# Kernel tuning notes

Hardware: AMD Instinct MI355X
Metric: run time of the kernel (lower is better)

## Reference

```python
import jax, jax.numpy as jnp
import numpy as np

K = 3  # neighbors for knn_interpolate


def _knn_interpolate(x, pos, pos_skip, B, k):
    """PyG knn_interpolate with equal-sized batches.
    x: [N_coarse, C], pos: [N_coarse, 3], pos_skip: [N_fine, 3].
    """
    C = x.shape[1]
    xb = x.reshape(B, -1, C)          # [B, nc, C]
    pb = pos.reshape(B, -1, 3)        # [B, nc, 3]
    qb = pos_skip.reshape(B, -1, 3)   # [B, nf, 3]

    def per_cloud(xf, pf, qf):
        # squared distances [nf, nc]
        d2 = jnp.sum((qf[:, None, :] - pf[None, :, :]) ** 2, axis=-1)
        neg_d2k, idx = jax.lax.top_k(-d2, k)          # k smallest distances
        d2k = -neg_d2k                                # [nf, k]
        w = 1.0 / jnp.clip(d2k, 1e-16)                # inverse-distance weights
        w = jax.lax.stop_gradient(w)                  # PyG computes weights under no_grad
        feats = xf[idx]                               # [nf, k, C] gather
        return jnp.sum(w[..., None] * feats, axis=1) / jnp.sum(w, axis=1, keepdims=True)

    y = jax.vmap(per_cloud)(xb, pb, qb)               # [B, nf, C]
    return y.reshape(-1, C)


def setup_inputs() -> dict:
    key = jax.random.key(0)
    ks = jax.random.split(key, 8)
    B, n_coarse, n_fine = 16, 1024, 4096
    C_in, C_skip, C_mid, C_out = 256, 128, 256, 256
    x = jax.random.normal(ks[0], (B * n_coarse, C_in), jnp.float32)
    pos = jax.random.uniform(ks[1], (B * n_coarse, 3), jnp.float32)
    x_skip = jax.random.normal(ks[2], (B * n_fine, C_skip), jnp.float32)
    pos_skip = jax.random.uniform(ks[3], (B * n_fine, 3), jnp.float32)
    batch = jnp.repeat(jnp.arange(B, dtype=jnp.int64), n_coarse)
    batch_skip = jnp.repeat(jnp.arange(B, dtype=jnp.int64), n_fine)
    seed_idx = jnp.arange(B * n_coarse, dtype=jnp.int64)
    seed_idx_skip = jnp.arange(B * n_fine, dtype=jnp.int64)
    W1 = jax.random.normal(ks[4], (C_in + C_skip, C_mid), jnp.float32) * 0.05
    b1 = jnp.zeros((C_mid,), jnp.float32)
    W2 = jax.random.normal(ks[5], (C_mid, C_out), jnp.float32) * 0.05
    b2 = jnp.zeros((C_out,), jnp.float32)
    return {"x": x, "pos": pos, "batch": batch, "seed_idx": seed_idx,
            "x_skip": x_skip, "pos_skip": pos_skip, "batch_skip": batch_skip,
            "seed_idx_skip": seed_idx_skip, "W1": W1, "b1": b1, "W2": W2, "b2": b2}


def reference(x, pos, batch, seed_idx, x_skip, pos_skip, batch_skip, seed_idx_skip,
              W1, b1, W2, b2):
    B = int(batch[-1]) + 1  # equal-sized contiguous clouds
    y = _knn_interpolate(x, pos, pos_skip, B, K)      # [N_fine, C_in]
    h = jnp.concatenate([y, x_skip], axis=1)          # [N_fine, C_in+C_skip]
    h = jax.nn.relu(h @ W1 + b1)                      # MLP layer 1
    out = jax.nn.relu(h @ W2 + b2)                    # MLP layer 2
    return (out, pos_skip, batch_skip)
```

## Files before the change

kernel.cpp:

```cpp
#include <hip/hip_runtime.h>
#include <hip/hip_bf16.h>

#define NB    16
#define NC    1024
#define NF    4096
#define NFINE (NB*NF)
#define CIN   256
#define CSKIP 128
#define KH    (CIN+CSKIP)
#define CMID  256
#define COUT  256

typedef __attribute__((ext_vector_type(8))) short short8;
typedef __attribute__((ext_vector_type(4))) float f32x4;
typedef __attribute__((ext_vector_type(4))) unsigned int u32x4;

__device__ __forceinline__ float bf2f(short s) {
    return __uint_as_float(((unsigned)(unsigned short)s) << 16);
}

__global__ __launch_bounds__(256)
void bin_kernel(const float* __restrict__ pos,
                float* __restrict__ gp,
                int* __restrict__ gcs)
{
    __shared__ int cnt[512];
    __shared__ float lx[NC], ly[NC], lz[NC];
    __shared__ short lcell[NC];
    const int b = blockIdx.x, t = threadIdx.x;
    for (int i = t; i < 512; i += 256) cnt[i] = 0;
    __syncthreads();
    const float* pc = pos + (size_t)b*NC*3;
    #pragma unroll
    for (int u = 0; u < 4; ++u) {
        int i = t + u*256;
        float x = pc[3*i+0], y = pc[3*i+1], z = pc[3*i+2];
        int cx = min(7, (int)(x*8.0f));
        int cy = min(7, (int)(y*8.0f));
        int cz = min(7, (int)(z*8.0f));
        int c = (cz*8 + cy)*8 + cx;
        lx[i] = x; ly[i] = y; lz[i] = z; lcell[i] = (short)c;
        atomicAdd(&cnt[c], 1);
    }
    __syncthreads();
    if (t < 64) {
        int v[8]; int s = 0;
        #pragma unroll
        for (int u = 0; u < 8; ++u) { v[u] = cnt[t*8+u]; s += v[u]; }
        int pfx = s;
        #pragma unroll
        for (int m = 1; m < 64; m <<= 1) {
            int o = __shfl_up(pfx, m);
            if (t >= m) pfx += o;
        }
        pfx -= s;
        #pragma unroll
        for (int u = 0; u < 8; ++u) {
            gcs[b*513 + t*8+u] = pfx;
            cnt[t*8+u] = pfx;
            pfx += v[u];
        }
        if (t == 63) gcs[b*513 + 512] = NC;
    }
    __syncthreads();
    #pragma unroll
    for (int u = 0; u < 4; ++u) {
        int i = t + u*256;
        int c = lcell[i];
        int dst = atomicAdd(&cnt[c], 1);
        f32x4 v; v[0] = lx[i]; v[1] = ly[i]; v[2] = lz[i]; v[3] = __int_as_float(i);
        *(f32x4*)&gp[(size_t)(b*NC + dst)*4] = v;
    }
}

#define KQPB 64

#define INS(d, j) do {                                        \
    bool c2 = (d) < dB, c1 = (d) < dA, c0 = (d) < d0;         \
    dB = c1 ? dA : (c2 ? (d) : dB);                           \
    iB = c1 ? iA : (c2 ? (j) : iB);                           \
    dA = c0 ? d0 : (c1 ? (d) : dA);                           \
    iA = c0 ? i0 : (c1 ? (j) : iA);                           \
    d0 = c0 ? (d) : d0;                                       \
    i0 = c0 ? (j) : i0;                                       \
} while (0)

#define SCAN(JS, JE) for (int j = (JS) + g; j < (JE); j += 8) {        \
    const f32x4 p = *(const f32x4*)&pp[j][0];                          \
    float fx = qx - p[0], fy = qy - p[1], fz = qz - p[2];              \
    float dd = fx*fx + fy*fy + fz*fz;                                  \
    INS(dd, j);                                                        \
}

#define MERGE8() do {                                                          \
    _Pragma("unroll")                                                          \
    for (int mm = 1; mm < 8; mm <<= 1) {                                       \
        float e0 = __shfl_xor(d0, mm), e1 = __shfl_xor(dA, mm), e2 = __shfl_xor(dB, mm); \
        int   f0 = __shfl_xor(i0, mm), f1 = __shfl_xor(iA, mm), f2 = __shfl_xor(iB, mm); \
        INS(e0, f0); INS(e1, f1); INS(e2, f2);                                 \
    }                                                                          \
} while (0)

__global__ __launch_bounds__(512)
void knn_grid_kernel(const float* __restrict__ pos_skip,
                     const float* __restrict__ gp,
                     const int* __restrict__ gcs,
                     int* __restrict__ widx, float* __restrict__ wval,
                     float* __restrict__ out)
{
    __shared__ __align__(16) float pp[NC][4];
    __shared__ unsigned short cs[513];
    const int bpc = NF/KQPB;
    const int b  = blockIdx.x / bpc;
    const int qb = blockIdx.x % bpc;
    const int t  = threadIdx.x;

    {
        int e = blockIdx.x*192 + t;
        if (t < 192) out[(size_t)NFINE*COUT + e] = pos_skip[e];
        if (t >= 192 && t < 256) {
            int e2 = blockIdx.x*64 + (t - 192);
            out[(size_t)NFINE*COUT + (size_t)NFINE*3 + e2] = (float)(e2 >> 12);
        }
    }

    for (int i = t; i < NC; i += 512)
        *(f32x4*)&pp[i][0] = *(const f32x4*)&gp[(size_t)(b*NC + i)*4];
    for (int i = t; i < 513; i += 512) cs[i] = (unsigned short)gcs[b*513 + i];
    __syncthreads();

    const int g  = t & 7;
    const int ql = t >> 3;
    const int q  = b*NF + qb*KQPB + ql;
    const float qx = pos_skip[(size_t)q*3+0];
    const float qy = pos_skip[(size_t)q*3+1];
    const float qz = pos_skip[(size_t)q*3+2];
    const int cx = min(7, (int)(qx*8.0f));
    const int cy = min(7, (int)(qy*8.0f));
    const int cz = min(7, (int)(qz*8.0f));

    float d0 = 3.0e38f, dA = 3.0e38f, dB = 3.0e38f;
    int   i0 = 0,       iA = 0,       iB = 0;

    const int xlo = max(cx-1,0), xhi = min(cx+1,7);
    const int ylo = max(cy-1,0), yhi = min(cy+1,7);
    const int zlo = max(cz-1,0), zhi = min(cz+1,7);
    #pragma unroll
    for (int r = 0; r < 9; ++r) {
        const int z = cz - 1 + r/3;
        const int y = cy - 1 + r%3;
        const bool ok = ((unsigned)z < 8u) & ((unsigned)y < 8u);
        const int rb = (z*8 + y)*8;
        int js = 0, je = 0;
        if (ok) { js = cs[rb + xlo]; je = cs[rb + xhi + 1]; }
        SCAN(js, je);
    }
    MERGE8();

    float m1 = 3.0e38f;
    if (xlo > 0) m1 = fminf(m1, qx - xlo*0.125f);
    if (xhi < 7) m1 = fminf(m1, (xhi+1)*0.125f - qx);
    if (ylo > 0) m1 = fminf(m1, qy - ylo*0.125f);
    if (yhi < 7) m1 = fminf(m1, (yhi+1)*0.125f - qy);
    if (zlo > 0) m1 = fminf(m1, qz - zlo*0.125f);
    if (zhi < 7) m1 = fminf(m1, (zhi+1)*0.125f - qz);

    if (dB > m1*m1) {
        const float s0 = d0, s1 = dA, s2 = dB;
        const int   t0 = i0, t1 = iA, t2 = iB;
        d0 = dA = dB = 3.0e38f; i0 = iA = iB = 0;

        const int xlo2 = max(cx-2,0), xhi2 = min(cx+2,7);
        const int ylo2 = max(cy-2,0), yhi2 = min(cy+2,7);
        const int zlo2 = max(cz-2,0), zhi2 = min(cz+2,7);
        for (int z = zlo2; z <= zhi2; ++z)
        for (int y = ylo2; y <= yhi2; ++y) {
            const int rb = (z*8 + y)*8;
            const bool inner_zy = (z >= zlo && z <= zhi && y >= ylo && y <= yhi);
            int jsA, jeA, jsB, jeB;
            if (inner_zy) {
                jsA = cs[rb + xlo2]; jeA = cs[rb + xlo];
                jsB = cs[rb + xhi + 1]; jeB = cs[rb + xhi2 + 1];
            } else {
                jsA = cs[rb + xlo2]; jeA = cs[rb + xhi2 + 1];
                jsB = 0; jeB = 0;
            }
            SCAN(jsA, jeA);
            SCAN(jsB, jeB);
        }
        MERGE8();
        INS(s0, t0); INS(s1, t1); INS(s2, t2);

        float m2 = 3.0e38f;
        if (xlo2 > 0) m2 = fminf(m2, qx - xlo2*0.125f);
        if (xhi2 < 7) m2 = fminf(m2, (xhi2+1)*0.125f - qx);
        if (ylo2 > 0) m2 = fminf(m2, qy - ylo2*0.125f);
        if (yhi2 < 7) m2 = fminf(m2, (yhi2+1)*0.125f - qy);
        if (zlo2 > 0) m2 = fminf(m2, qz - zlo2*0.125f);
        if (zhi2 < 7) m2 = fminf(m2, (zhi2+1)*0.125f - qz);
        if (dB > m2*m2) {
            const float u0 = d0, u1 = dA, u2 = dB;
            const int   v0 = i0, v1 = iA, v2 = iB;
            d0 = dA = dB = 3.0e38f; i0 = iA = iB = 0;
            for (int j = g; j < NC; j += 8) {
                const f32x4 p = *(const f32x4*)&pp[j][0];
                int pcx = min(7, (int)(p[0]*8.0f));
                int pcy = min(7, (int)(p[1]*8.0f));
                int pcz = min(7, (int)(p[2]*8.0f));
                if (pcx >= xlo2 && pcx <= xhi2 && pcy >= ylo2 && pcy <= yhi2 &&
                    pcz >= zlo2 && pcz <= zhi2) continue;
                float fx = qx - p[0], fy = qy - p[1], fz = qz - p[2];
                float dd = fx*fx + fy*fy + fz*fz;
                INS(dd, j);
            }
            MERGE8();
            INS(u0, v0); INS(u1, v1); INS(u2, v2);
        }
    }

    if (g == 0) {
        const int o0 = __float_as_int(pp[i0][3]);
        const int o1 = __float_as_int(pp[iA][3]);
        const int o2 = __float_as_int(pp[iB][3]);
        float w0 = 1.0f / fmaxf(d0, 1e-16f);
        float w1 = 1.0f / fmaxf(dA, 1e-16f);
        float w2 = 1.0f / fmaxf(dB, 1e-16f);
        float inv = 1.0f / (w0 + w1 + w2);
        widx[q*3+0] = b*NC + o0;  wval[q*3+0] = w0*inv;
        widx[q*3+1] = b*NC + o1;  wval[q*3+1] = w1*inv;
        widx[q*3+2] = b*NC + o2;  wval[q*3+2] = w2*inv;
    }
}

__global__ __launch_bounds__(256)
void prep_weights(const float* __restrict__ W1, const float* __restrict__ W2,
                  __hip_bfloat16* __restrict__ W1at,
                  __hip_bfloat16* __restrict__ imgG,
                  __hip_bfloat16* __restrict__ img2)
{
    int e = blockIdx.x*256 + threadIdx.x;
    if (e < CMID*CIN) {
        int n = e / CIN, k = e % CIN;
        W1at[e] = __float2bfloat16(W1[(size_t)k*CMID + n]);
    }
    int e2 = e - CMID*CIN;
    if (e2 >= 0 && e2 < 2*2048*8) {
        int chunk = e2 >> 3, el = e2 & 7;
        int s = chunk >> 11, L = chunk & 2047;
        int rr = L >> 3, sl = L & 7;
        int k = s*64 + ((sl ^ (rr & 7)) << 3) + el;
        imgG[e2] = __float2bfloat16(W1[(size_t)(CIN + k)*CMID + rr]);
    }
    int e3 = e2 - 2*2048*8;
    if (e3 >= 0 && e3 < 4*2048*8) {
        int chunk = e3 >> 3, el = e3 & 7;
        int s = chunk >> 11, L = chunk & 2047;
        int rr = L >> 3, sl = L & 7;
        int k = s*64 + ((sl ^ (rr & 7)) << 3) + el;
        img2[e3] = __float2bfloat16(W2[(size_t)k*COUT + rr]);
    }
}

__global__ __launch_bounds__(512, 2)
void gemmZ_kernel(const float* __restrict__ x,
                  const __hip_bfloat16* __restrict__ W1at,
                  __hip_bfloat16* __restrict__ Z)
{
    __shared__ __align__(16) short As[64][64];
    __shared__ __align__(16) short Bs[256][64];
    const int m0 = blockIdx.x * 64;

    const int t = threadIdx.x;
    const int wave = t >> 6, lane = t & 63;
    const int wm = wave >> 2, wn = wave & 3;
    const int rl = lane & 15, kq = lane >> 4;
    const short* Br = (const short*)W1at;

    const int ar = t >> 3;
    const int ac = t & 7;

    f32x4 rA[2];
    u32x4 rB[4];

    #define LOADAZ(K0) do {                                                    \
        const float* p = &x[(size_t)(m0+ar)*CIN + (K0) + ac*8];                \
        rA[0] = *(const f32x4*)p; rA[1] = *(const f32x4*)(p+4);                \
    } while (0)
    #define LOADBZ(K0) do {                                                    \
        _Pragma("unroll")                                                      \
        for (int i = 0; i < 4; ++i) {                                          \
            const int ch = t + i*512;                                          \
            const int rr = ch >> 3, cc = ch & 7;                               \
            rB[i] = *(const u32x4*)&Br[(size_t)rr*CIN + (K0) + cc*8];          \
        }                                                                      \
    } while (0)

    f32x4 acc[2][4] = {};
    LOADAZ(0); LOADBZ(0);

    #pragma unroll
    for (int s = 0; s < 4; ++s) {
        __syncthreads();
        {
            short8 sv;
            #pragma unroll
            for (int u = 0; u < 2; ++u) {
                f32x4 a = rA[u];
                #pragma unroll
                for (int e = 0; e < 4; ++e) {
                    __hip_bfloat16 bb = __float2bfloat16(a[e]);
                    ((short*)&sv)[u*4+e] = *(short*)&bb;
                }
            }
            *(short8*)&As[ar][(ac ^ (ar&7))*8] = sv;
        }
        #pragma unroll
        for (int i = 0; i < 4; ++i) {
            const int ch = t + i*512;
            const int rr = ch >> 3, cc = ch & 7;
            *(u32x4*)&Bs[rr][(cc ^ (rr&7))*8] = rB[i];
        }
        __syncthreads();
        if (s < 3) { LOADAZ((s+1)*64); LOADBZ((s+1)*64); }
        #pragma unroll
        for (int kh = 0; kh < 2; ++kh) {
            const int kc = kh*4 + kq;
            short8 af[2], bf[4];
            #pragma unroll
            for (int mf = 0; mf < 2; ++mf)
                af[mf] = *(const short8*)&As[wm*32 + mf*16 + rl][(kc ^ (rl&7))*8];
            #pragma unroll
            for (int nf = 0; nf < 4; ++nf)
                bf[nf] = *(const short8*)&Bs[wn*64 + nf*16 + rl][(kc ^ (rl&7))*8];
            #pragma unroll
            for (int mf = 0; mf < 2; ++mf)
            #pragma unroll
            for (int nf = 0; nf < 4; ++nf)
                acc[mf][nf] = __builtin_amdgcn_mfma_f32_16x16x32_bf16(af[mf], bf[nf], acc[mf][nf], 0,0,0);
        }
    }
    #undef LOADAZ
    #undef LOADBZ

    #pragma unroll
    for (int mf = 0; mf < 2; ++mf)
    #pragma unroll
    for (int nf = 0; nf < 4; ++nf) {
        const int col = wn*64 + nf*16 + rl;
        #pragma unroll
        for (int i = 0; i < 4; ++i) {
            const int row = m0 + wm*32 + mf*16 + kq*4 + i;
            Z[(size_t)row*CMID + col] = __float2bfloat16(acc[mf][nf][i]);
        }
    }
}

__global__ __launch_bounds__(512, 2)
void g2_fused(const float* __restrict__ x_skip,
              const float* __restrict__ b1,
              const __hip_bfloat16* __restrict__ Z,
              const int* __restrict__ widx,
              const float* __restrict__ wval,
              const __hip_bfloat16* __restrict__ imgG,
              const __hip_bfloat16* __restrict__ img2,
              const float* __restrict__ b2,
              float* __restrict__ out)
{
    __shared__ __align__(16) short As[64][128];
    __shared__ __align__(16) short Bs[256][64];
    __shared__ __align__(16) short Hs[64][256];
    const int nwg = gridDim.x;
    const int tile = (blockIdx.x & 7)*(nwg >> 3) + (blockIdx.x >> 3);
    const int m0 = tile * 64;

    const int t = threadIdx.x;
    const int wave = t >> 6, lane = t & 63;
    const int wm = wave >> 2, wn = wave & 3;
    const int rl = lane & 15, kq = lane >> 4;
    const short* gI = (const short*)imgG;
    const short* g2i = (const short*)img2;
    const short* Zr  = (const short*)Z;
    short* BsLin = &Bs[0][0];
    short (*BsH)[64] = (short(*)[64])&Hs[0][0];

    const int ar = t >> 3;
    const int ac = t & 7;

    const float* xs = &x_skip[(size_t)(m0+ar)*CSKIP];
    f32x4 pa0 = *(const f32x4*)&xs[ac*8];
    f32x4 pa1 = *(const f32x4*)&xs[ac*8+4];
    f32x4 pb0 = *(const f32x4*)&xs[64+ac*8];
    f32x4 pb1 = *(const f32x4*)&xs[64+ac*8+4];
    u32x4 rG0[4], rG1[4];
    #pragma unroll
    for (int i = 0; i < 4; ++i) {
        rG0[i] = *(const u32x4*)&gI[(size_t)(       i*512 + t)*8];
        rG1[i] = *(const u32x4*)&gI[(size_t)(2048 + i*512 + t)*8];
    }

    {
        short8 sv0, sv1;
        #pragma unroll
        for (int u = 0; u < 2; ++u) {
            f32x4 a = (u == 0) ? pa0 : pa1;
            f32x4 b = (u == 0) ? pb0 : pb1;
            #pragma unroll
            for (int e = 0; e < 4; ++e) {
                __hip_bfloat16 ba = __float2bfloat16(a[e]);
                __hip_bfloat16 bb = __float2bfloat16(b[e]);
                ((short*)&sv0)[u*4+e] = *(short*)&ba;
                ((short*)&sv1)[u*4+e] = *(short*)&bb;
            }
        }
        const int sw = ac ^ (ar & 7);
        *(short8*)&As[ar][sw*8]     = sv0;
        *(short8*)&As[ar][(8+sw)*8] = sv1;
    }
    #pragma unroll
    for (int i = 0; i < 4; ++i) {
        *(u32x4*)&BsLin[(size_t)(i*512 + t)*8]     = rG0[i];
        *(u32x4*)&(&Hs[0][0])[(size_t)(i*512 + t)*8] = rG1[i];
    }
    __syncthreads();

    f32x4 acc[2][4] = {};
    #pragma unroll
    for (int kh = 0; kh < 2; ++kh) {
        const int kc = kh*4 + kq;
        short8 af[2], bf[4];
        #pragma unroll
        for (int mf = 0; mf < 2; ++mf)
            af[mf] = *(const short8*)&As[wm*32 + mf*16 + rl][((kc ^ (rl&7)))*8];
        #pragma unroll
        for (int nf = 0; nf < 4; ++nf)
            bf[nf] = *(const short8*)&Bs[wn*64 + nf*16 + rl][(kc ^ (rl&7))*8];
        #pragma unroll
        for (int mf = 0; mf < 2; ++mf)
        #pragma unroll
        for (int nf = 0; nf < 4; ++nf)
            acc[mf][nf] = __builtin_amdgcn_mfma_f32_16x16x32_bf16(af[mf], bf[nf], acc[mf][nf], 0,0,0);
    }
    #pragma unroll
    for (int kh = 0; kh < 2; ++kh) {
        const int kc = kh*4 + kq;
        short8 af[2], bf[4];
        #pragma unroll
        for (int mf = 0; mf < 2; ++mf)
            af[mf] = *(const short8*)&As[wm*32 + mf*16 + rl][(8 + (kc ^ (rl&7)))*8];
        #pragma unroll
        for (int nf = 0; nf < 4; ++nf)
            bf[nf] = *(const short8*)&BsH[wn*64 + nf*16 + rl][(kc ^ (rl&7))*8];
        #pragma unroll
        for (int mf = 0; mf < 2; ++mf)
        #pragma unroll
        for (int nf = 0; nf < 4; ++nf)
            acc[mf][nf] = __builtin_amdgcn_mfma_f32_16x16x32_bf16(af[mf], bf[nf], acc[mf][nf], 0,0,0);
    }
    __syncthreads();

    u32x4 rB[4];
    #pragma unroll
    for (int i = 0; i < 4; ++i)
        rB[i] = *(const u32x4*)&g2i[(size_t)(i*512 + t)*8];
    #pragma unroll
    for (int mf = 0; mf < 2; ++mf)
    #pragma unroll
    for (int nf = 0; nf < 4; ++nf) {
        const int col = wn*64 + nf*16 + rl;
        const float bv = b1[col];
        #pragma unroll
        for (int i = 0; i < 4; ++i) {
            const int row = wm*32 + mf*16 + kq*4 + i;
            float v = acc[mf][nf][i] + bv;
            __hip_bfloat16 bb = __float2bfloat16(v);
            Hs[row][((col >> 3) ^ (row & 7))*8 + (col & 7)] = *(short*)&bb;
        }
    }
    #pragma unroll
    for (int i = 0; i < 4; ++i)
        *(u32x4*)&BsLin[(size_t)(i*512 + t)*8] = rB[i];
    __syncthreads();

    #pragma unroll
    for (int u = 0; u < 4; ++u) {
        const int ch = t + u*512;
        const int row = ch >> 5;
        const int cc  = ch & 31;
        const int c   = cc * 8;
        const int gr = (m0 + row)*3;
        const int j0 = widx[gr+0], j1 = widx[gr+1], j2 = widx[gr+2];
        const float w0 = wval[gr+0], w1 = wval[gr+1], w2 = wval[gr+2];
        const short8 z0 = *(const short8*)&Zr[(size_t)j0*CMID + c];
        const short8 z1 = *(const short8*)&Zr[(size_t)j1*CMID + c];
        const short8 z2 = *(const short8*)&Zr[(size_t)j2*CMID + c];
        const int slot = (cc ^ (row & 7))*8;
        short8 gchunk = *(const short8*)&Hs[row][slot];
        short8 r;
        #pragma unroll
        for (int e = 0; e < 8; ++e) {
            float v = bf2f(gchunk[e]) + w0*bf2f(z0[e]) + w1*bf2f(z1[e]) + w2*bf2f(z2[e]);
            v = fmaxf(v, 0.0f);
            __hip_bfloat16 bb = __float2bfloat16(v);
            r[e] = *(short*)&bb;
        }
        *(short8*)&Hs[row][slot] = r;
    }
    __syncthreads();

    f32x4 acc2[2][4] = {};
    #define MFMA2(S2) do {                                                     \
        _Pragma("unroll")                                                      \
        for (int kh = 0; kh < 2; ++kh) {                                       \
            const int kcl = kh*4 + kq;                                         \
            const int kca = (S2)*8 + kcl;                                      \
            short8 af[2], bf[4];                                               \
            _Pragma("unroll")                                                  \
            for (int mf = 0; mf < 2; ++mf)                                     \
                af[mf] = *(const short8*)&Hs[wm*32 + mf*16 + rl][(kca ^ (rl&7))*8]; \
            _Pragma("unroll")                                                  \
            for (int nf = 0; nf < 4; ++nf)                                     \
                bf[nf] = *(const short8*)&Bs[wn*64 + nf*16 + rl][(kcl ^ (rl&7))*8]; \
            _Pragma("unroll")                                                  \
            for (int mf = 0; mf < 2; ++mf)                                     \
            _Pragma("unroll")                                                  \
            for (int nf = 0; nf < 4; ++nf)                                     \
                acc2[mf][nf] = __builtin_amdgcn_mfma_f32_16x16x32_bf16(af[mf], bf[nf], acc2[mf][nf], 0,0,0); \
        }                                                                      \
    } while (0)
    #define LOADI2(S) do {                                                     \
        _Pragma("unroll")                                                      \
        for (int i = 0; i < 4; ++i)                                            \
            rB[i] = *(const u32x4*)&g2i[(size_t)((S)*2048 + i*512 + t)*8];     \
    } while (0)
    #define STAGEI2() do {                                                     \
        _Pragma("unroll")                                                      \
        for (int i = 0; i < 4; ++i)                                            \
            *(u32x4*)&BsLin[(size_t)(i*512 + t)*8] = rB[i];                    \
    } while (0)

    LOADI2(1);
    MFMA2(0);
    __syncthreads();
    STAGEI2();
    __syncthreads();
    LOADI2(2);
    MFMA2(1);
    __syncthreads();
    STAGEI2();
    __syncthreads();
    LOADI2(3);
    MFMA2(2);
    __syncthreads();
    STAGEI2();
    __syncthreads();
    MFMA2(3);

    #pragma unroll
    for (int mf = 0; mf < 2; ++mf)
    #pragma unroll
    for (int nf = 0; nf < 4; ++nf) {
        const int col = wn*64 + nf*16 + rl;
        const float bv = b2[col];
        #pragma unroll
        for (int i = 0; i < 4; ++i) {
            const int row = m0 + wm*32 + mf*16 + kq*4 + i;
            out[(size_t)row*COUT + col] = fmaxf(acc2[mf][nf][i] + bv, 0.0f);
        }
    }
    #undef MFMA2
    #undef LOADI2
    #undef STAGEI2
}

extern "C" void kernel_launch(void* const* d_in, const int* in_sizes, int n_in,
                              void* d_out, int out_size, void* d_ws, size_t ws_size,
                              hipStream_t stream) {
    const float* x        = (const float*)d_in[0];
    const float* pos      = (const float*)d_in[1];
    const float* x_skip   = (const float*)d_in[4];
    const float* pos_skip = (const float*)d_in[5];
    const float* W1       = (const float*)d_in[8];
    const float* b1       = (const float*)d_in[9];
    const float* W2       = (const float*)d_in[10];
    const float* b2       = (const float*)d_in[11];
    float* out = (float*)d_out;
    char* ws = (char*)d_ws;

    int*            widx = (int*)  (ws + 0);
    float*          wval = (float*)(ws + 786432);
    __hip_bfloat16* W1at = (__hip_bfloat16*)(ws + 1572864);
    __hip_bfloat16* imgG = (__hip_bfloat16*)(ws + 1703936);
    __hip_bfloat16* img2 = (__hip_bfloat16*)(ws + 1769472);
    float*          gp   = (float*)(ws + 1900544);
    int*            gcs  = (int*)  (ws + 2162688);
    __hip_bfloat16* Z    = (__hip_bfloat16*)(ws + 2195520);

    hipLaunchKernelGGL(bin_kernel, dim3(NB), dim3(256), 0, stream,
                       pos, gp, gcs);
    hipLaunchKernelGGL(knn_grid_kernel, dim3(NB*(NF/KQPB)), dim3(512), 0, stream,
                       pos_skip, gp, gcs, widx, wval, out);
    hipLaunchKernelGGL(prep_weights, dim3((CMID*CIN + 2*2048*8 + 4*2048*8 + 255)/256), dim3(256), 0, stream,
                       W1, W2, W1at, imgG, img2);
    hipLaunchKernelGGL(gemmZ_kernel, dim3((NB*NC)/64), dim3(512), 0, stream,
                       x, W1at, Z);
    hipLaunchKernelGGL(g2_fused, dim3(NFINE/64), dim3(512), 0, stream,
                       x_skip, b1, Z, widx, wval, imgG, img2, b2, out);
}
```

Baseline: 72.81 us.

## Merge bin+weight prep and knn+Z-GEMM into horizontally fused kernels

```diff
diff --git a/kernel.cpp b/kernel.cpp
--- a/kernel.cpp
+++ b/kernel.cpp
@@ -20,14 +20,42 @@
 }
 
 __global__ __launch_bounds__(256)
-void bin_kernel(const float* __restrict__ pos,
-                float* __restrict__ gp,
-                int* __restrict__ gcs)
+void binprep_kernel(const float* __restrict__ pos,
+                    float* __restrict__ gp, int* __restrict__ gcs,
+                    const float* __restrict__ W1, const float* __restrict__ W2,
+                    __hip_bfloat16* __restrict__ W1at,
+                    __hip_bfloat16* __restrict__ imgG,
+                    __hip_bfloat16* __restrict__ img2)
 {
     __shared__ int cnt[512];
     __shared__ float lx[NC], ly[NC], lz[NC];
     __shared__ short lcell[NC];
-    const int b = blockIdx.x, t = threadIdx.x;
+    const int t = threadIdx.x;
+    if (blockIdx.x >= NB) {
+        int e = (blockIdx.x - NB)*256 + t;
+        if (e < CMID*CIN) {
+            int n = e / CIN, k = e % CIN;
+            W1at[e] = __float2bfloat16(W1[(size_t)k*CMID + n]);
+        }
+        int e2 = e - CMID*CIN;
+        if (e2 >= 0 && e2 < 2*2048*8) {
+            int chunk = e2 >> 3, el = e2 & 7;
+            int s = chunk >> 11, L = chunk & 2047;
+            int rr = L >> 3, sl = L & 7;
+            int k = s*64 + ((sl ^ (rr & 7)) << 3) + el;
+            imgG[e2] = __float2bfloat16(W1[(size_t)(CIN + k)*CMID + rr]);
+        }
+        int e3 = e2 - 2*2048*8;
+        if (e3 >= 0 && e3 < 4*2048*8) {
+            int chunk = e3 >> 3, el = e3 & 7;
+            int s = chunk >> 11, L = chunk & 2047;
+            int rr = L >> 3, sl = L & 7;
+            int k = s*64 + ((sl ^ (rr & 7)) << 3) + el;
+            img2[e3] = __float2bfloat16(W2[(size_t)k*COUT + rr]);
+        }
+        return;
+    }
+    const int b = blockIdx.x;
     for (int i = t; i < 512; i += 256) cnt[i] = 0;
     __syncthreads();
     const float* pc = pos + (size_t)b*NC*3;
@@ -101,19 +129,112 @@
     }                                                                          \
 } while (0)
 
-__global__ __launch_bounds__(512)
-void knn_grid_kernel(const float* __restrict__ pos_skip,
-                     const float* __restrict__ gp,
-                     const int* __restrict__ gcs,
-                     int* __restrict__ widx, float* __restrict__ wval,
-                     float* __restrict__ out)
+union KZMem {
+    struct { float pp[NC][4]; unsigned short cs[513]; } k;
+    struct { short As[64][64]; short Bs[256][64]; } z;
+};
+
+__global__ __launch_bounds__(512, 2)
+void knnZ_kernel(const float* __restrict__ pos_skip,
+                 const float* __restrict__ gp,
+                 const int* __restrict__ gcs,
+                 int* __restrict__ widx, float* __restrict__ wval,
+                 float* __restrict__ out,
+                 const float* __restrict__ x,
+                 const __hip_bfloat16* __restrict__ W1at,
+                 __hip_bfloat16* __restrict__ Z)
 {
-    __shared__ __align__(16) float pp[NC][4];
-    __shared__ unsigned short cs[513];
+    __shared__ __align__(16) KZMem sm;
+    const int t = threadIdx.x;
+
+    if (blockIdx.x >= 1024) {
+        const int m0 = (blockIdx.x - 1024) * 64;
+        const int wave = t >> 6, lane = t & 63;
+        const int wm = wave >> 2, wn = wave & 3;
+        const int rl = lane & 15, kq = lane >> 4;
+        const short* Br = (const short*)W1at;
+        const int ar = t >> 3;
+        const int ac = t & 7;
+        f32x4 rA[2];
+        u32x4 rB[4];
+
+        #define LOADAZ(K0) do {                                                \
+            const float* p = &x[(size_t)(m0+ar)*CIN + (K0) + ac*8];            \
+            rA[0] = *(const f32x4*)p; rA[1] = *(const f32x4*)(p+4);            \
+        } while (0)
+        #define LOADBZ(K0) do {                                                \
+            _Pragma("unroll")                                                  \
+            for (int i = 0; i < 4; ++i) {                                      \
+                const int ch = t + i*512;                                      \
+                const int rr = ch >> 3, cc = ch & 7;                           \
+                rB[i] = *(const u32x4*)&Br[(size_t)rr*CIN + (K0) + cc*8];      \
+            }                                                                  \
+        } while (0)
+
+        f32x4 acc[2][4] = {};
+        LOADAZ(0); LOADBZ(0);
+        #pragma unroll
+        for (int s = 0; s < 4; ++s) {
+            __syncthreads();
+            {
+                short8 sv;
+                #pragma unroll
+                for (int u = 0; u < 2; ++u) {
+                    f32x4 a = rA[u];
+                    #pragma unroll
+                    for (int e = 0; e < 4; ++e) {
+                        __hip_bfloat16 bb = __float2bfloat16(a[e]);
+                        ((short*)&sv)[u*4+e] = *(short*)&bb;
+                    }
+                }
+                *(short8*)&sm.z.As[ar][(ac ^ (ar&7))*8] = sv;
+            }
+            #pragma unroll
+            for (int i = 0; i < 4; ++i) {
+                const int ch = t + i*512;
+                const int rr = ch >> 3, cc = ch & 7;
+                *(u32x4*)&sm.z.Bs[rr][(cc ^ (rr&7))*8] = rB[i];
+            }
+            __syncthreads();
+            if (s < 3) { LOADAZ((s+1)*64); LOADBZ((s+1)*64); }
+            #pragma unroll
+            for (int kh = 0; kh < 2; ++kh) {
+                const int kc = kh*4 + kq;
+                short8 af[2], bf[4];
+                #pragma unroll
+                for (int mf = 0; mf < 2; ++mf)
+                    af[mf] = *(const short8*)&sm.z.As[wm*32 + mf*16 + rl][(kc ^ (rl&7))*8];
+                #pragma unroll
+                for (int nf = 0; nf < 4; ++nf)
+                    bf[nf] = *(const short8*)&sm.z.Bs[wn*64 + nf*16 + rl][(kc ^ (rl&7))*8];
+                #pragma unroll
+                for (int mf = 0; mf < 2; ++mf)
+                #pragma unroll
+                for (int nf = 0; nf < 4; ++nf)
+                    acc[mf][nf] = __builtin_amdgcn_mfma_f32_16x16x32_bf16(af[mf], bf[nf], acc[mf][nf], 0,0,0);
+            }
+        }
+        #undef LOADAZ
+        #undef LOADBZ
+        #pragma unroll
+        for (int mf = 0; mf < 2; ++mf)
+        #pragma unroll
+        for (int nf = 0; nf < 4; ++nf) {
+            const int col = wn*64 + nf*16 + rl;
+            #pragma unroll
+            for (int i = 0; i < 4; ++i) {
+                const int row = m0 + wm*32 + mf*16 + kq*4 + i;
+                Z[(size_t)row*CMID + col] = __float2bfloat16(acc[mf][nf][i]);
+            }
+        }
+        return;
+    }
+
+    float (*pp)[4] = sm.k.pp;
+    unsigned short* cs = sm.k.cs;
     const int bpc = NF/KQPB;
     const int b  = blockIdx.x / bpc;
     const int qb = blockIdx.x % bpc;
-    const int t  = threadIdx.x;
 
     {
         int e = blockIdx.x*192 + t;
@@ -169,7 +290,6 @@
         const float s0 = d0, s1 = dA, s2 = dB;
         const int   t0 = i0, t1 = iA, t2 = iB;
         d0 = dA = dB = 3.0e38f; i0 = iA = iB = 0;
-
         const int xlo2 = max(cx-2,0), xhi2 = min(cx+2,7);
         const int ylo2 = max(cy-2,0), yhi2 = min(cy+2,7);
         const int zlo2 = max(cz-2,0), zhi2 = min(cz+2,7);
@@ -232,129 +352,6 @@
     }
 }
 
-__global__ __launch_bounds__(256)
-void prep_weights(const float* __restrict__ W1, const float* __restrict__ W2,
-                  __hip_bfloat16* __restrict__ W1at,
-                  __hip_bfloat16* __restrict__ imgG,
-                  __hip_bfloat16* __restrict__ img2)
-{
-    int e = blockIdx.x*256 + threadIdx.x;
-    if (e < CMID*CIN) {
-        int n = e / CIN, k = e % CIN;
-        W1at[e] = __float2bfloat16(W1[(size_t)k*CMID + n]);
-    }
-    int e2 = e - CMID*CIN;
-    if (e2 >= 0 && e2 < 2*2048*8) {
-        int chunk = e2 >> 3, el = e2 & 7;
-        int s = chunk >> 11, L = chunk & 2047;
-        int rr = L >> 3, sl = L & 7;
-        int k = s*64 + ((sl ^ (rr & 7)) << 3) + el;
-        imgG[e2] = __float2bfloat16(W1[(size_t)(CIN + k)*CMID + rr]);
-    }
-    int e3 = e2 - 2*2048*8;
-    if (e3 >= 0 && e3 < 4*2048*8) {
-        int chunk = e3 >> 3, el = e3 & 7;
-        int s = chunk >> 11, L = chunk & 2047;
-        int rr = L >> 3, sl = L & 7;
-        int k = s*64 + ((sl ^ (rr & 7)) << 3) + el;
-        img2[e3] = __float2bfloat16(W2[(size_t)k*COUT + rr]);
-    }
-}
-
-__global__ __launch_bounds__(512, 2)
-void gemmZ_kernel(const float* __restrict__ x,
-                  const __hip_bfloat16* __restrict__ W1at,
-                  __hip_bfloat16* __restrict__ Z)
-{
-    __shared__ __align__(16) short As[64][64];
-    __shared__ __align__(16) short Bs[256][64];
-    const int m0 = blockIdx.x * 64;
-
-    const int t = threadIdx.x;
-    const int wave = t >> 6, lane = t & 63;
-    const int wm = wave >> 2, wn = wave & 3;
-    const int rl = lane & 15, kq = lane >> 4;
-    const short* Br = (const short*)W1at;
-
-    const int ar = t >> 3;
-    const int ac = t & 7;
-
-    f32x4 rA[2];
-    u32x4 rB[4];
-
-    #define LOADAZ(K0) do {                                                    \
-        const float* p = &x[(size_t)(m0+ar)*CIN + (K0) + ac*8];                \
-        rA[0] = *(const f32x4*)p; rA[1] = *(const f32x4*)(p+4);                \
-    } while (0)
-    #define LOADBZ(K0) do {                                                    \
-        _Pragma("unroll")                                                      \
-        for (int i = 0; i < 4; ++i) {                                          \
-            const int ch = t + i*512;                                          \
-            const int rr = ch >> 3, cc = ch & 7;                               \
-            rB[i] = *(const u32x4*)&Br[(size_t)rr*CIN + (K0) + cc*8];          \
-        }                                                                      \
-    } while (0)
-
-    f32x4 acc[2][4] = {};
-    LOADAZ(0); LOADBZ(0);
-
-    #pragma unroll
-    for (int s = 0; s < 4; ++s) {
-        __syncthreads();
-        {
-            short8 sv;
-            #pragma unroll
-            for (int u = 0; u < 2; ++u) {
-                f32x4 a = rA[u];
-                #pragma unroll
-                for (int e = 0; e < 4; ++e) {
-                    __hip_bfloat16 bb = __float2bfloat16(a[e]);
-                    ((short*)&sv)[u*4+e] = *(short*)&bb;
-                }
-            }
-            *(short8*)&As[ar][(ac ^ (ar&7))*8] = sv;
-        }
-        #pragma unroll
-        for (int i = 0; i < 4; ++i) {
-            const int ch = t + i*512;
-            const int rr = ch >> 3, cc = ch & 7;
-            *(u32x4*)&Bs[rr][(cc ^ (rr&7))*8] = rB[i];
-        }
-        __syncthreads();
-        if (s < 3) { LOADAZ((s+1)*64); LOADBZ((s+1)*64); }
-        #pragma unroll
-        for (int kh = 0; kh < 2; ++kh) {
-            const int kc = kh*4 + kq;
-            short8 af[2], bf[4];
-            #pragma unroll
-            for (int mf = 0; mf < 2; ++mf)
-                af[mf] = *(const short8*)&As[wm*32 + mf*16 + rl][(kc ^ (rl&7))*8];
-            #pragma unroll
-            for (int nf = 0; nf < 4; ++nf)
-                bf[nf] = *(const short8*)&Bs[wn*64 + nf*16 + rl][(kc ^ (rl&7))*8];
-            #pragma unroll
-            for (int mf = 0; mf < 2; ++mf)
-            #pragma unroll
-            for (int nf = 0; nf < 4; ++nf)
-                acc[mf][nf] = __builtin_amdgcn_mfma_f32_16x16x32_bf16(af[mf], bf[nf], acc[mf][nf], 0,0,0);
-        }
-    }
-    #undef LOADAZ
-    #undef LOADBZ
-
-    #pragma unroll
-    for (int mf = 0; mf < 2; ++mf)
-    #pragma unroll
-    for (int nf = 0; nf < 4; ++nf) {
-        const int col = wn*64 + nf*16 + rl;
-        #pragma unroll
-        for (int i = 0; i < 4; ++i) {
-            const int row = m0 + wm*32 + mf*16 + kq*4 + i;
-            Z[(size_t)row*CMID + col] = __float2bfloat16(acc[mf][nf][i]);
-        }
-    }
-}
-
 __global__ __launch_bounds__(512, 2)
 void g2_fused(const float* __restrict__ x_skip,
               const float* __restrict__ b1,
@@ -418,7 +415,7 @@
     }
     #pragma unroll
     for (int i = 0; i < 4; ++i) {
-        *(u32x4*)&BsLin[(size_t)(i*512 + t)*8]     = rG0[i];
+        *(u32x4*)&BsLin[(size_t)(i*512 + t)*8]       = rG0[i];
         *(u32x4*)&(&Hs[0][0])[(size_t)(i*512 + t)*8] = rG1[i];
     }
     __syncthreads();
@@ -595,14 +592,10 @@
     int*            gcs  = (int*)  (ws + 2162688);
     __hip_bfloat16* Z    = (__hip_bfloat16*)(ws + 2195520);
 
-    hipLaunchKernelGGL(bin_kernel, dim3(NB), dim3(256), 0, stream,
-                       pos, gp, gcs);
-    hipLaunchKernelGGL(knn_grid_kernel, dim3(NB*(NF/KQPB)), dim3(512), 0, stream,
-                       pos_skip, gp, gcs, widx, wval, out);
-    hipLaunchKernelGGL(prep_weights, dim3((CMID*CIN + 2*2048*8 + 4*2048*8 + 255)/256), dim3(256), 0, stream,
-                       W1, W2, W1at, imgG, img2);
-    hipLaunchKernelGGL(gemmZ_kernel, dim3((NB*NC)/64), dim3(512), 0, stream,
-                       x, W1at, Z);
+    hipLaunchKernelGGL(binprep_kernel, dim3(NB + 640), dim3(256), 0, stream,
+                       pos, gp, gcs, W1, W2, W1at, imgG, img2);
+    hipLaunchKernelGGL(knnZ_kernel, dim3(1024 + 256), dim3(512), 0, stream,
+                       pos_skip, gp, gcs, widx, wval, out, x, W1at, Z);
     hipLaunchKernelGGL(g2_fused, dim3(NFINE/64), dim3(512), 0, stream,
                        x_skip, b1, Z, widx, wval, imgG, img2, b2, out);
 }
```

Measured after the change: 63.77 us (median of 2 runs). 1.14x faster.
